# Kernel optimization log

Hardware: AMD Instinct MI355X
Metric: run time of the kernel (lower is better)

The kernel has to match this reference:

```python
import jax, jax.numpy as jnp
import numpy as np

N, D = 4096, 2048

def setup_inputs() -> dict:
    key = jax.random.key(0)
    k1, k2 = jax.random.split(key)
    Ws = jax.random.normal(k1, (N, D), dtype=jnp.float32)
    # nn.Bilinear(D, D, 1): weight [1, D, D], bias [1]
    W = jax.random.normal(k2, (1, D, D), dtype=jnp.float32) * (1.0 / np.sqrt(D))
    b = jnp.zeros((1,), dtype=jnp.float32)
    return {"Ws": Ws, "W": W, "b": b}

def reference(Ws, W, b):
    # A[i, j] = Ws[i] @ W[0] @ Ws[j] + b[0]  (bilinear score for every pair)
    t = Ws @ W[0]                 # [N, D]
    A = t @ Ws.T + b[0]           # [N, N]
    return jax.nn.softmax(A, axis=1)
```

## Files before the change

### kernel.cpp

```cpp
#include <hip/hip_runtime.h>

typedef __bf16 bf16x8 __attribute__((ext_vector_type(8)));
typedef float f32x4 __attribute__((ext_vector_type(4)));
typedef unsigned short u16;
typedef u16 u16x8 __attribute__((ext_vector_type(8)));

#define AS1 __attribute__((address_space(1)))
#define AS3 __attribute__((address_space(3)))

__device__ __forceinline__ void split2(float x, u16& h, u16& l) {
  __bf16 hb = (__bf16)x;
  float hf = (float)hb;
  __bf16 lb = (__bf16)(x - hf);
  h = __builtin_bit_cast(u16, hb);
  l = __builtin_bit_cast(u16, lb);
}

__global__ __launch_bounds__(256) void k_pack_ws(const float* __restrict__ X,
                                                 u16* __restrict__ P) {
  const int total8 = (4096 * 2048) / 8;
  for (int idx = blockIdx.x * 256 + threadIdx.x; idx < total8; idx += gridDim.x * 256) {
    int row = idx >> 8;
    int k8  = idx & 255;
    const float* src = X + ((size_t)row << 11) + (k8 << 3);
    const float4 v0 = *(const float4*)src;
    const float4 v1 = *(const float4*)(src + 4);
    float xv[8] = {v0.x, v0.y, v0.z, v0.w, v1.x, v1.y, v1.z, v1.w};
    u16x8 hv, lv;
#pragma unroll
    for (int j = 0; j < 8; ++j) { u16 h, l; split2(xv[j], h, l); hv[j] = h; lv[j] = l; }
    size_t base = ((size_t)row << 12) + (size_t)((k8 >> 2) << 6) + ((k8 & 3) << 3);
    *(u16x8*)(P + base) = hv;
    *(u16x8*)(P + base + 32) = lv;
  }
}

__global__ __launch_bounds__(256) void k_transpose_pack_w(const float* __restrict__ W,
                                                          u16* __restrict__ P) {
  __shared__ float tile[32][33];
  const int tx = threadIdx.x, ty = threadIdx.y;
  const int kbase = blockIdx.y << 5, cbase = blockIdx.x << 5;
#pragma unroll
  for (int i = 0; i < 4; ++i)
    tile[ty * 4 + i][tx] = W[((size_t)(kbase + ty * 4 + i) << 11) + cbase + tx];
  __syncthreads();
#pragma unroll
  for (int i = 0; i < 4; ++i) {
    int c = cbase + ty * 4 + i;
    float v = tile[tx][ty * 4 + i];
    u16 h, l; split2(v, h, l);
    size_t base = ((size_t)c << 12) + (size_t)(kbase << 1) + tx;
    P[base] = h;
    P[base + 32] = l;
  }
}

template <bool SPLIT_OUT>
__global__ __launch_bounds__(256, 2) void k_gemm_nt(const u16* __restrict__ Ap,
                                                    const u16* __restrict__ Bp,
                                                    float* __restrict__ Cout,
                                                    u16* __restrict__ Cpack,
                                                    const int Ncols) {
  __shared__ __align__(16) u16 lds_a[128 * 64];
  __shared__ __align__(16) u16 lds_b[128 * 64];
  const int tid = threadIdx.x;
  const int lane = tid & 63, w = tid >> 6;
  const int wr = w >> 1, wc = w & 1;
  const int row0 = blockIdx.y << 7, col0 = blockIdx.x << 7;
  const int lrow = lane & 15, kg = lane >> 4;

  f32x4 acc[4][4] = {};

  const u16* abase = Ap + ((size_t)row0 << 12);
  const u16* bbase = Bp + ((size_t)col0 << 12);

  int offAh[4], offAl[4], offBh[4], offBl[4];
#pragma unroll
  for (int m = 0; m < 4; ++m) {
    int r = wr * 64 + m * 16 + lrow;
    int sw = r & 7;
    offAh[m] = r * 64 + ((kg ^ sw) << 3);
    offAl[m] = r * 64 + (((4 + kg) ^ sw) << 3);
    int rb = wc * 64 + m * 16 + lrow;
    int swb = rb & 7;
    offBh[m] = rb * 64 + ((kg ^ swb) << 3);
    offBl[m] = rb * 64 + (((4 + kg) ^ swb) << 3);
  }

  for (int kb = 0; kb < 64; ++kb) {
    const int kofs = kb << 6;
#pragma unroll
    for (int i = 0; i < 4; ++i) {
      int s = i * 256 + tid;
      int r = s >> 3, c = s & 7;
      int cs = c ^ (r & 7);
      __builtin_amdgcn_global_load_lds(
          (const AS1 unsigned int*)(abase + ((size_t)r << 12) + kofs + (cs << 3)),
          (AS3 unsigned int*)(lds_a + ((i * 256 + w * 64) << 3)), 16, 0, 0);
    }
#pragma unroll
    for (int i = 0; i < 4; ++i) {
      int s = i * 256 + tid;
      int r = s >> 3, c = s & 7;
      int cs = c ^ (r & 7);
      __builtin_amdgcn_global_load_lds(
          (const AS1 unsigned int*)(bbase + ((size_t)r << 12) + kofs + (cs << 3)),
          (AS3 unsigned int*)(lds_b + ((i * 256 + w * 64) << 3)), 16, 0, 0);
    }
    __syncthreads();

    bf16x8 ah[4], al[4];
#pragma unroll
    for (int m = 0; m < 4; ++m) {
      ah[m] = *(const bf16x8*)&lds_a[offAh[m]];
      al[m] = *(const bf16x8*)&lds_a[offAl[m]];
    }
#pragma unroll
    for (int n = 0; n < 4; ++n) {
      bf16x8 bh = *(const bf16x8*)&lds_b[offBh[n]];
      bf16x8 bl = *(const bf16x8*)&lds_b[offBl[n]];
#pragma unroll
      for (int m = 0; m < 4; ++m) {
        acc[m][n] = __builtin_amdgcn_mfma_f32_16x16x32_bf16(ah[m], bh, acc[m][n], 0, 0, 0);
        acc[m][n] = __builtin_amdgcn_mfma_f32_16x16x32_bf16(ah[m], bl, acc[m][n], 0, 0, 0);
        acc[m][n] = __builtin_amdgcn_mfma_f32_16x16x32_bf16(al[m], bh, acc[m][n], 0, 0, 0);
      }
    }
    __syncthreads();
  }

#pragma unroll
  for (int m = 0; m < 4; ++m) {
#pragma unroll
    for (int n = 0; n < 4; ++n) {
#pragma unroll
      for (int j = 0; j < 4; ++j) {
        int gr = row0 + wr * 64 + m * 16 + kg * 4 + j;
        int gc = col0 + wc * 64 + n * 16 + lrow;
        float x = acc[m][n][j];
        if (SPLIT_OUT) {
          u16 h, l; split2(x, h, l);
          size_t base = ((size_t)gr << 12) + (size_t)((gc >> 5) << 6) + (gc & 31);
          Cpack[base] = h;
          Cpack[base + 32] = l;
        } else {
          Cout[(size_t)gr * Ncols + gc] = x;
        }
      }
    }
  }
}

__global__ __launch_bounds__(256) void k_softmax_rows(float* __restrict__ A) {
  const int row = blockIdx.x;
  float* p = A + ((size_t)row << 12);
  const int tid = threadIdx.x;
  const int lane = tid & 63, w = tid >> 6;
  float4 v[4];
  float mx = -3.0e38f;
#pragma unroll
  for (int i = 0; i < 4; ++i) {
    v[i] = ((const float4*)p)[tid + (i << 8)];
    mx = fmaxf(mx, fmaxf(fmaxf(v[i].x, v[i].y), fmaxf(v[i].z, v[i].w)));
  }
#pragma unroll
  for (int off = 32; off; off >>= 1) mx = fmaxf(mx, __shfl_xor(mx, off, 64));
  __shared__ float redm[4], reds[4];
  if (lane == 0) redm[w] = mx;
  __syncthreads();
  mx = fmaxf(fmaxf(redm[0], redm[1]), fmaxf(redm[2], redm[3]));
  float s = 0.f;
#pragma unroll
  for (int i = 0; i < 4; ++i) {
    v[i].x = __expf(v[i].x - mx);
    v[i].y = __expf(v[i].y - mx);
    v[i].z = __expf(v[i].z - mx);
    v[i].w = __expf(v[i].w - mx);
    s += (v[i].x + v[i].y) + (v[i].z + v[i].w);
  }
#pragma unroll
  for (int off = 32; off; off >>= 1) s += __shfl_xor(s, off, 64);
  if (lane == 0) reds[w] = s;
  __syncthreads();
  s = (reds[0] + reds[1]) + (reds[2] + reds[3]);
  const float inv = 1.0f / s;
#pragma unroll
  for (int i = 0; i < 4; ++i) {
    v[i].x *= inv; v[i].y *= inv; v[i].z *= inv; v[i].w *= inv;
    ((float4*)p)[tid + (i << 8)] = v[i];
  }
}

extern "C" void kernel_launch(void* const* d_in, const int* in_sizes, int n_in,
                              void* d_out, int out_size, void* d_ws, size_t ws_size,
                              hipStream_t stream) {
  (void)in_sizes; (void)n_in; (void)out_size; (void)ws_size;
  const float* Ws = (const float*)d_in[0];
  const float* W  = (const float*)d_in[1];
  float* out = (float*)d_out;

  u16* ws_pack = (u16*)d_ws;
  u16* wt_pack = ws_pack + (size_t)4096 * 4096;
  u16* t_pack  = wt_pack + (size_t)2048 * 4096;

  k_pack_ws<<<4096, 256, 0, stream>>>(Ws, ws_pack);
  k_transpose_pack_w<<<dim3(64, 64), dim3(32, 8), 0, stream>>>(W, wt_pack);
  k_gemm_nt<true><<<dim3(16, 32), 256, 0, stream>>>(ws_pack, wt_pack, nullptr, t_pack, 2048);
  k_gemm_nt<false><<<dim3(32, 32), 256, 0, stream>>>(t_pack, ws_pack, out, nullptr, 4096);
  k_softmax_rows<<<4096, 256, 0, stream>>>(out);
}
```

Baseline: 284.7 us.

## Replace second GEMM with double-buffered 256x256 tile, 8-wave kernel

Adds a new GEMM kernel for the large N x N product that uses 256x256 output tiles with 512 threads and 8 waves. It double-buffers LDS so the global->LDS loads for tile t+2 overlap the MFMA work on tile t, using explicit waitcnt and barriers, and raises wave priority around the MFMA blocks. The larger tile is meant to improve operand reuse and cut per-K-step stalls. In exchange it uses 128KB of LDS and 128 accumulator floats per thread, and the grid drops to 256 blocks, which limits occupancy and may leave some CUs idle.

```diff
diff --git a/kernel.cpp b/kernel.cpp
--- a/kernel.cpp
+++ b/kernel.cpp
@@ -151,6 +151,119 @@
   }
 }
 
+__global__ __launch_bounds__(512, 2) void k_gemm256(const u16* __restrict__ Ap,
+                                                    const u16* __restrict__ Bp,
+                                                    float* __restrict__ Cout) {
+  __shared__ __align__(16) u16 sm[4 * 16384];
+  const int tid = threadIdx.x;
+  const int lane = tid & 63, w = tid >> 6;
+  const int wr = w >> 2, wc = w & 3;
+  const int row0 = blockIdx.y << 8, col0 = blockIdx.x << 8;
+  const int lrow = lane & 15, kg = lane >> 4;
+  const int sw = lrow & 7;
+
+  const u16* Abase = Ap + ((size_t)row0 << 12);
+  const u16* Bbase = Bp + ((size_t)col0 << 12);
+
+  size_t gsrc[4];
+  int dsto[4];
+#pragma unroll
+  for (int i = 0; i < 4; ++i) {
+    int s = i * 512 + tid;
+    int r = s >> 3, c = s & 7;
+    int cs = c ^ (r & 7);
+    gsrc[i] = ((size_t)r << 12) + (cs << 3);
+    dsto[i] = (i * 512 + w * 64) << 3;
+  }
+
+  const int baseAh = (wr * 128 + lrow) * 64 + ((kg ^ sw) << 3);
+  const int baseAl = (wr * 128 + lrow) * 64 + (((4 | kg) ^ sw) << 3);
+  const int baseBh = (wc * 64 + lrow) * 64 + ((kg ^ sw) << 3);
+  const int baseBl = (wc * 64 + lrow) * 64 + (((4 | kg) ^ sw) << 3);
+
+  f32x4 acc[8][4] = {};
+
+  auto stage = [&](int t, u16* la, u16* lb) {
+    const int kofs = t << 6;
+#pragma unroll
+    for (int i = 0; i < 4; ++i)
+      __builtin_amdgcn_global_load_lds((const AS1 unsigned int*)(Abase + gsrc[i] + kofs),
+                                       (AS3 unsigned int*)(la + dsto[i]), 16, 0, 0);
+#pragma unroll
+    for (int i = 0; i < 4; ++i)
+      __builtin_amdgcn_global_load_lds((const AS1 unsigned int*)(Bbase + gsrc[i] + kofs),
+                                       (AS3 unsigned int*)(lb + dsto[i]), 16, 0, 0);
+  };
+
+  stage(0, sm, sm + 16384);
+  stage(1, sm + 32768, sm + 49152);
+  asm volatile("s_waitcnt vmcnt(8)" ::: "memory");
+  __builtin_amdgcn_sched_barrier(0);
+  __builtin_amdgcn_s_barrier();
+
+  for (int t = 0; t < 64; ++t) {
+    u16* la = sm + (t & 1) * 32768;
+    u16* lb = la + 16384;
+    bf16x8 bh[4], bl[4];
+#pragma unroll
+    for (int p = 0; p < 4; ++p) {
+      if (p == 0) {
+#pragma unroll
+        for (int n = 0; n < 4; ++n) {
+          bh[n] = *(const bf16x8*)&lb[baseBh + n * 1024];
+          bl[n] = *(const bf16x8*)&lb[baseBl + n * 1024];
+        }
+      }
+      bf16x8 ah0 = *(const bf16x8*)&la[baseAh + (2 * p) * 1024];
+      bf16x8 al0 = *(const bf16x8*)&la[baseAl + (2 * p) * 1024];
+      bf16x8 ah1 = *(const bf16x8*)&la[baseAh + (2 * p + 1) * 1024];
+      bf16x8 al1 = *(const bf16x8*)&la[baseAl + (2 * p + 1) * 1024];
+      __builtin_amdgcn_s_setprio(1);
+#pragma unroll
+      for (int n = 0; n < 4; ++n) {
+        acc[2 * p][n]     = __builtin_amdgcn_mfma_f32_16x16x32_bf16(ah0, bh[n], acc[2 * p][n], 0, 0, 0);
+        acc[2 * p + 1][n] = __builtin_amdgcn_mfma_f32_16x16x32_bf16(ah1, bh[n], acc[2 * p + 1][n], 0, 0, 0);
+      }
+#pragma unroll
+      for (int n = 0; n < 4; ++n) {
+        acc[2 * p][n]     = __builtin_amdgcn_mfma_f32_16x16x32_bf16(ah0, bl[n], acc[2 * p][n], 0, 0, 0);
+        acc[2 * p + 1][n] = __builtin_amdgcn_mfma_f32_16x16x32_bf16(ah1, bl[n], acc[2 * p + 1][n], 0, 0, 0);
+      }
+#pragma unroll
+      for (int n = 0; n < 4; ++n) {
+        acc[2 * p][n]     = __builtin_amdgcn_mfma_f32_16x16x32_bf16(al0, bh[n], acc[2 * p][n], 0, 0, 0);
+        acc[2 * p + 1][n] = __builtin_amdgcn_mfma_f32_16x16x32_bf16(al1, bh[n], acc[2 * p + 1][n], 0, 0, 0);
+      }
+      __builtin_amdgcn_s_setprio(0);
+      if (p < 3) __builtin_amdgcn_s_barrier();
+    }
+    asm volatile("s_waitcnt lgkmcnt(0)" ::: "memory");
+    __builtin_amdgcn_sched_barrier(0);
+    __builtin_amdgcn_s_barrier();
+    if (t + 2 < 64) {
+      stage(t + 2, la, lb);
+      asm volatile("s_waitcnt vmcnt(8)" ::: "memory");
+    } else {
+      asm volatile("s_waitcnt vmcnt(0)" ::: "memory");
+    }
+    __builtin_amdgcn_sched_barrier(0);
+    __builtin_amdgcn_s_barrier();
+  }
+
+#pragma unroll
+  for (int m = 0; m < 8; ++m) {
+#pragma unroll
+    for (int n = 0; n < 4; ++n) {
+#pragma unroll
+      for (int j = 0; j < 4; ++j) {
+        int gr = row0 + wr * 128 + m * 16 + kg * 4 + j;
+        int gc = col0 + wc * 64 + n * 16 + lrow;
+        Cout[((size_t)gr << 12) + gc] = acc[m][n][j];
+      }
+    }
+  }
+}
+
 __global__ __launch_bounds__(256) void k_softmax_rows(float* __restrict__ A) {
   const int row = blockIdx.x;
   float* p = A + ((size_t)row << 12);
@@ -206,6 +319,6 @@
   k_pack_ws<<<4096, 256, 0, stream>>>(Ws, ws_pack);
   k_transpose_pack_w<<<dim3(64, 64), dim3(32, 8), 0, stream>>>(W, wt_pack);
   k_gemm_nt<true><<<dim3(16, 32), 256, 0, stream>>>(ws_pack, wt_pack, nullptr, t_pack, 2048);
-  k_gemm_nt<false><<<dim3(32, 32), 256, 0, stream>>>(t_pack, ws_pack, out, nullptr, 4096);
+  k_gemm256<<<dim3(16, 16), 512, 0, stream>>>(t_pack, ws_pack, out);
   k_softmax_rows<<<4096, 256, 0, stream>>>(out);
 }
```

New measurement: 278.6 us. 1.02x faster.
